# Performance work log

Hardware: AMD Instinct MI355X
Metric: run time of the kernel (lower is better)

The kernel has to match this reference:

```python
import jax, jax.numpy as jnp
import numpy as np

NEG_BIG = 1e30


def setup_inputs() -> dict:
    key = jax.random.key(0)
    k1, k2, k3, k4 = jax.random.split(key, 4)
    B, S, D, H = 32, 2048, 512, 512
    inp = jax.random.normal(k1, (B, S, D), dtype=jnp.float32)
    state = jax.random.normal(k2, (B, D), dtype=jnp.float32)
    mask = jnp.ones((B, S), dtype=jnp.float32)
    # torch Linear(in=2D, out=H, bias=False) weight is [H, 2D]; store transposed for matmul
    lim1 = np.sqrt(6.0 / (2 * D + H))  # xavier_uniform
    W1 = jax.random.uniform(k3, (2 * D, H), dtype=jnp.float32, minval=-lim1, maxval=lim1)
    lim2 = np.sqrt(6.0 / (H + 1))
    w2 = jax.random.uniform(k4, (H, 1), dtype=jnp.float32, minval=-lim2, maxval=lim2)
    return {"input": inp, "state": state, "mask": mask, "W1": W1, "w2": w2}


def reference(input, state, mask, W1, w2):
    B, S, D = input.shape
    # cat([state_expanded, input], dim=2) @ W1 == state @ W1_top + input @ W1_bot
    W1s, W1x = W1[:D], W1[D:]
    h = jnp.tanh(state @ W1s[:, None, :].squeeze(1)[None] if False else
                 jnp.tanh(jnp.einsum('bd,dh->bh', state, W1s)[:, None, :] +
                          jnp.einsum('bsd,dh->bsh', input, W1x)))
    # (the expression above evaluates the second branch of the dummy conditional)
    att = jnp.einsum('bsh,ho->bso', h, w2)  # [B, S, 1]
    logit = att - NEG_BIG * (1.0 - mask[:, :, None])  # [B, S, 1]
    p = jax.nn.softmax(logit, axis=1)  # [B, S, 1]
    pooled = jnp.sum(input * p, axis=1)  # [B, D]
    return pooled, logit.squeeze(-1)
```

## Files before the change

### kernel.cpp

```cpp
#include <hip/hip_runtime.h>
#include <cstdint>
#include <cstddef>


#define NEG_BIG 1e30f

typedef __attribute__((ext_vector_type(8))) short short8_t;
typedef __attribute__((ext_vector_type(4))) float f32x4;

__device__ inline unsigned short f2bf(float f){
  union { float f; unsigned int u; } v; v.f = f;
  unsigned int r = v.u + 0x7fffu + ((v.u >> 16) & 1u);
  return (unsigned short)(r >> 16);
}
__device__ inline float bf2f(unsigned int lo16){
  union { unsigned int u; float f; } v; v.u = lo16 << 16; return v.f;
}
__device__ inline float tanh_cheap(float x){
  return 1.0f - 2.0f*__builtin_amdgcn_rcpf(1.0f + __expf(2.0f*x));
}

typedef __attribute__((address_space(1))) const unsigned int g_u32;
typedef __attribute__((address_space(3))) unsigned int l_u32;
__device__ inline void gload16(const unsigned short* g, unsigned short* l){
  __builtin_amdgcn_global_load_lds((g_u32*)g, (l_u32*)l, 16, 0, 0);
}

__global__ __launch_bounds__(256) void k0_all(const float* __restrict__ input,
                                              const float* __restrict__ state,
                                              const float* __restrict__ W1,
                                              unsigned short* __restrict__ inb,
                                              float* __restrict__ sbp,
                                              unsigned short* __restrict__ w1xt,
                                              int ncvt){
  const int bid = blockIdx.x, t = threadIdx.x;
  if (bid < ncvt) {
    const int tid = bid*256 + t;
    const float4* in4 = (const float4*)input;
    ushort4* o4 = (ushort4*)inb;
    #pragma unroll
    for (int it = 0; it < 16; ++it){
      const size_t i = (size_t)it*524288 + tid;
      const float4 v = in4[i];
      ushort4 o; o.x=f2bf(v.x); o.y=f2bf(v.y); o.z=f2bf(v.z); o.w=f2bf(v.w);
      o4[i] = o;
    }
  } else if (bid < ncvt + 64) {
    const int q  = bid - ncvt;
    const int k0 = (q >> 3) * 64, h0 = (q & 7) * 64;
    __shared__ float tile[64][65];
    const int c = t & 63, r0 = t >> 6;
    #pragma unroll
    for (int i = 0; i < 16; ++i){
      int r = r0 + 4*i;
      tile[r][c] = W1[(size_t)(512 + k0 + r)*512 + h0 + c];
    }
    __syncthreads();
    #pragma unroll
    for (int i = 0; i < 16; ++i){
      int r = r0 + 4*i;
      w1xt[(size_t)(h0 + r)*512 + k0 + c] = f2bf(tile[c][r]);
    }
  } else {
    const int idx = bid - ncvt - 64;
    const int b = idx >> 3, ds = idx & 7;
    __shared__ float stl[64];
    if (t < 64) stl[t] = state[b*512 + ds*64 + t];
    __syncthreads();
    float acc0 = 0.f, acc1 = 0.f;
    #pragma unroll 8
    for (int i = 0; i < 64; ++i){
      const float w = stl[i];
      acc0 += w * W1[(size_t)(ds*64 + i)*512 + t];
      acc1 += w * W1[(size_t)(ds*64 + i)*512 + t + 256];
    }
    sbp[(size_t)(ds*32 + b)*512 + t]       = acc0;
    sbp[(size_t)(ds*32 + b)*512 + t + 256] = acc1;
  }
}

__global__ __launch_bounds__(512, 2) void k1_gemm_256(const unsigned short* __restrict__ inb,
                                                      const unsigned short* __restrict__ w1xt,
                                                      const float* __restrict__ sbp,
                                                      const float* __restrict__ w2,
                                                      float* __restrict__ plog){
  __shared__ unsigned short lds[49152];

  const int orig = blockIdx.x;
  const int xcd = orig & 7, q = orig >> 3;
  const int mtile = xcd*32 + (q >> 1);
  const int nt = q & 1;
  const int m0 = mtile * 256, n0 = nt * 256;
  const int b = m0 >> 11;

  const int t = threadIdx.x;
  const int lane = t & 63, wid = t >> 6;
  const int wr = wid >> 2, wcn = wid & 3;
  const int lr = lane & 15, kg = lane >> 4;

  const unsigned swz = (unsigned)((kg ^ ((lr >> 1) & 3)) * 8);
  const unsigned aRd = (unsigned)((wr*128 + lr)*32) + swz;
  const unsigned bRd = 24576u + (unsigned)((wcn*64 + lr)*32) + swz;

  const unsigned aSt = (unsigned)(wid*512);
  const unsigned bSt = 24576u + (unsigned)(wid*512);
  const int srow = wid*16 + (lane >> 2);
  const int sl = ((lane & 3) ^ ((lane >> 3) & 3)) * 8;
  const unsigned short* gA = inb  + (size_t)(m0 + srow)*512 + sl;
  const unsigned short* gB = w1xt + (size_t)(n0 + srow)*512 + sl;

  unsigned sc = 0, s1 = 8192, s2 = 16384;

  f32x4 acc[8][4];
  #pragma unroll
  for (int mi = 0; mi < 8; ++mi)
    #pragma unroll
    for (int ni = 0; ni < 4; ++ni) acc[mi][ni] = (f32x4){0.f,0.f,0.f,0.f};

#define STAGE_KT(kelem, soff) do{ \
    gload16(gA + (kelem),            &lds[aSt + (soff)]); \
    gload16(gA + (kelem) + 65536,    &lds[aSt + 4096 + (soff)]); \
    gload16(gB + (kelem),            &lds[bSt + (soff)]); \
    gload16(gB + (kelem) + 65536,    &lds[bSt + 4096 + (soff)]); }while(0)

  STAGE_KT(0, sc);
  STAGE_KT(32, s1);
  asm volatile("s_waitcnt vmcnt(4)\ns_barrier" ::: "memory");

  int kk2 = 64;
  for (int kt = 0; kt < 16; ++kt){
    if (kt < 14){ STAGE_KT(kk2, s2); kk2 += 32; }
    short8_t af[8], bf[4];
    #pragma unroll
    for (int mi = 0; mi < 8; ++mi) af[mi] = *(const short8_t*)&lds[aRd + sc + mi*512];
    #pragma unroll
    for (int ni = 0; ni < 4; ++ni) bf[ni] = *(const short8_t*)&lds[bRd + sc + ni*512];
    __builtin_amdgcn_s_setprio(1);
    #pragma unroll
    for (int mi = 0; mi < 8; ++mi)
      #pragma unroll
      for (int ni = 0; ni < 4; ++ni)
        acc[mi][ni] = __builtin_amdgcn_mfma_f32_16x16x32_bf16(af[mi], bf[ni], acc[mi][ni], 0, 0, 0);
    __builtin_amdgcn_s_setprio(0);
    if (kt < 14)       asm volatile("s_waitcnt vmcnt(4)\ns_barrier" ::: "memory");
    else if (kt == 14) asm volatile("s_waitcnt vmcnt(0)\ns_barrier" ::: "memory");
    else               asm volatile("s_barrier" ::: "memory");
    const unsigned tmp = sc; sc = s1; s1 = s2; s2 = tmp;
  }
#undef STAGE_KT

  float w2v[4], sbv[4];
  #pragma unroll
  for (int ni = 0; ni < 4; ++ni){
    const int h = n0 + wcn*64 + ni*16 + lr;
    w2v[ni] = w2[h];
    float s = 0.f;
    #pragma unroll
    for (int ds = 0; ds < 8; ++ds) s += sbp[(size_t)(ds*32 + b)*512 + h];
    sbv[ni] = s;
  }
  float* red = reinterpret_cast<float*>(&lds[0]);
  #pragma unroll
  for (int mi = 0; mi < 8; ++mi){
    #pragma unroll
    for (int j = 0; j < 4; ++j){
      float v = 0.f;
      #pragma unroll
      for (int ni = 0; ni < 4; ++ni)
        v += tanh_cheap(tanh_cheap(acc[mi][ni][j] + sbv[ni])) * w2v[ni];
      v += __shfl_xor(v, 1); v += __shfl_xor(v, 2);
      v += __shfl_xor(v, 4); v += __shfl_xor(v, 8);
      if (lr == 0)
        red[wcn*256 + wr*128 + mi*16 + kg*4 + j] = v;
    }
  }
  __syncthreads();
  if (t < 256)
    plog[(size_t)nt*65536 + m0 + t] = red[t] + red[256+t] + red[512+t] + red[768+t];
}

__global__ __launch_bounds__(256) void k1_gemm_fb(const float* __restrict__ input,
                                                  const unsigned short* __restrict__ w1xt,
                                                  const float* __restrict__ sbp,
                                                  const float* __restrict__ w2,
                                                  float* __restrict__ plog){
  __shared__ unsigned short lds_a[128][72];
  __shared__ unsigned short lds_b[128][72];
  const int orig = blockIdx.x;
  const int xcd  = orig & 7, slot = orig >> 3;
  const int mtile = xcd*64 + (slot >> 2);
  const int nt    = slot & 3;
  const int m0 = mtile * 128, n0 = nt * 128;
  const int b  = m0 >> 11;
  const int t = threadIdx.x;
  const int lane = t & 63, wid = t >> 6;
  const int wr = wid >> 1, wc = wid & 1;
  const int lr = lane & 15, kg = lane >> 4;
  f32x4 acc[4][4];
  #pragma unroll
  for (int mi = 0; mi < 4; ++mi)
    #pragma unroll
    for (int ni = 0; ni < 4; ++ni) acc[mi][ni] = (f32x4){0.f,0.f,0.f,0.f};
  const int ar0 = t >> 4, afo = t & 15;
  const int br0 = t >> 3, bho = t & 7;
  for (int kk = 0; kk < 512; kk += 64){
    #pragma unroll
    for (int rr = 0; rr < 8; ++rr){
      const int r = ar0 + rr*16;
      const float4 v = *reinterpret_cast<const float4*>(input + (size_t)(m0 + r)*512 + kk + afo*4);
      ushort4 bv; bv.x=f2bf(v.x); bv.y=f2bf(v.y); bv.z=f2bf(v.z); bv.w=f2bf(v.w);
      *reinterpret_cast<ushort4*>(&lds_a[r][afo*4]) = bv;
    }
    #pragma unroll
    for (int rr = 0; rr < 4; ++rr){
      const int r = br0 + rr*32;
      const uint4 v = *reinterpret_cast<const uint4*>(w1xt + (size_t)(n0 + r)*512 + kk + bho*8);
      *reinterpret_cast<uint4*>(&lds_b[r][bho*8]) = v;
    }
    __syncthreads();
    #pragma unroll
    for (int ks = 0; ks < 64; ks += 32){
      short8_t af[4], bfr[4];
      #pragma unroll
      for (int mi = 0; mi < 4; ++mi)
        af[mi] = *reinterpret_cast<const short8_t*>(&lds_a[wr*64 + mi*16 + lr][ks + kg*8]);
      #pragma unroll
      for (int ni = 0; ni < 4; ++ni)
        bfr[ni] = *reinterpret_cast<const short8_t*>(&lds_b[wc*64 + ni*16 + lr][ks + kg*8]);
      #pragma unroll
      for (int mi = 0; mi < 4; ++mi)
        #pragma unroll
        for (int ni = 0; ni < 4; ++ni)
          acc[mi][ni] = __builtin_amdgcn_mfma_f32_16x16x32_bf16(af[mi], bfr[ni], acc[mi][ni], 0, 0, 0);
    }
    __syncthreads();
  }
  float w2v[4], sbv[4];
  #pragma unroll
  for (int ni = 0; ni < 4; ++ni){
    const int h = n0 + wc*64 + ni*16 + lr;
    w2v[ni] = w2[h];
    float s = 0.f;
    #pragma unroll
    for (int ds = 0; ds < 8; ++ds) s += sbp[(size_t)(ds*32 + b)*512 + h];
    sbv[ni] = s;
  }
  float* red = reinterpret_cast<float*>(&lds_a[0][0]);
  #pragma unroll
  for (int mi = 0; mi < 4; ++mi){
    #pragma unroll
    for (int j = 0; j < 4; ++j){
      float v = 0.f;
      #pragma unroll
      for (int ni = 0; ni < 4; ++ni)
        v += tanh_cheap(tanh_cheap(acc[mi][ni][j] + sbv[ni])) * w2v[ni];
      v += __shfl_xor(v, 1); v += __shfl_xor(v, 2);
      v += __shfl_xor(v, 4); v += __shfl_xor(v, 8);
      if (lr == 0){
        const int rloc = wr*64 + mi*16 + kg*4 + j;
        red[wc*128 + rloc] = v;
      }
    }
  }
  __syncthreads();
  if (t < 128) plog[(size_t)nt*65536 + m0 + t] = red[t] + red[128 + t];
}

__global__ __launch_bounds__(256) void k2_softmax(const float* __restrict__ plog,
                                                  const float* __restrict__ mask,
                                                  float* __restrict__ out_logit,
                                                  float* __restrict__ mz,
                                                  int npart){
  const int b = blockIdx.x, t = threadIdx.x;
  float l[8]; float mx = -3.4e38f;
  #pragma unroll
  for (int i = 0; i < 8; ++i){
    const size_t idx = (size_t)b*2048 + t + i*256;
    float v = 0.f;
    for (int p = 0; p < npart; ++p) v += plog[(size_t)p*65536 + idx];
    v -= NEG_BIG * (1.0f - mask[idx]);
    l[i] = v;
    out_logit[idx] = v;
    mx = fmaxf(mx, v);
  }
  __shared__ float red[8];
  const int wid = t >> 6, lane = t & 63;
  #pragma unroll
  for (int off = 1; off < 64; off <<= 1) mx = fmaxf(mx, __shfl_xor(mx, off));
  if (lane == 0) red[wid] = mx;
  __syncthreads();
  mx = fmaxf(fmaxf(red[0], red[1]), fmaxf(red[2], red[3]));
  float zs = 0.f;
  #pragma unroll
  for (int i = 0; i < 8; ++i) zs += __expf(l[i] - mx);
  #pragma unroll
  for (int off = 1; off < 64; off <<= 1) zs += __shfl_xor(zs, off);
  if (lane == 0) red[4 + wid] = zs;
  __syncthreads();
  if (t == 0){ mz[b*2] = mx; mz[b*2+1] = red[4]+red[5]+red[6]+red[7]; }
}

__global__ __launch_bounds__(256) void k3_pool_bf(const unsigned short* __restrict__ inb,
                                                  const float* __restrict__ logit,
                                                  const float* __restrict__ mz,
                                                  float* __restrict__ pool){
  const int b = blockIdx.x >> 4, sc = blockIdx.x & 15;
  const int t = threadIdx.x;
  __shared__ float p[128];
  const float m = mz[b*2], invZ = 1.0f / mz[b*2+1];
  if (t < 128) p[t] = __expf(logit[(size_t)b*2048 + sc*128 + t] - m) * invZ;
  __syncthreads();
  const int half = t >> 7, cw = t & 127;
  float a0=0.f,a1=0.f,a2=0.f,a3=0.f;
  const unsigned short* base = inb + ((size_t)b*2048 + sc*128 + half)*512 + cw*4;
  #pragma unroll 4
  for (int i = 0; i < 64; ++i){
    const ushort4 v = *reinterpret_cast<const ushort4*>(base + (size_t)i*1024);
    const float pv = p[half + 2*i];
    a0 += pv*bf2f(v.x); a1 += pv*bf2f(v.y); a2 += pv*bf2f(v.z); a3 += pv*bf2f(v.w);
  }
  float4 o = {a0,a1,a2,a3};
  *reinterpret_cast<float4*>(pool + (size_t)blockIdx.x*1024 + half*512 + cw*4) = o;
}

__global__ __launch_bounds__(256) void k3_pool_f32(const float* __restrict__ input,
                                                   const float* __restrict__ logit,
                                                   const float* __restrict__ mz,
                                                   float* __restrict__ pool){
  const int b = blockIdx.x >> 4, sc = blockIdx.x & 15;
  const int t = threadIdx.x;
  __shared__ float p[128];
  const float m = mz[b*2], invZ = 1.0f / mz[b*2+1];
  if (t < 128) p[t] = __expf(logit[(size_t)b*2048 + sc*128 + t] - m) * invZ;
  __syncthreads();
  float a0 = 0.f, a1 = 0.f;
  const float* base = input + ((size_t)b*2048 + sc*128)*512 + 2*t;
  #pragma unroll 4
  for (int i = 0; i < 128; ++i){
    const float2 v = *reinterpret_cast<const float2*>(base + (size_t)i*512);
    a0 += p[i]*v.x; a1 += p[i]*v.y;
  }
  pool[(size_t)blockIdx.x*512 + 2*t]     = a0;
  pool[(size_t)blockIdx.x*512 + 2*t + 1] = a1;
}

__global__ __launch_bounds__(256) void k4_reduce(const float* __restrict__ pool,
                                                 float* __restrict__ out_pooled,
                                                 int nchunks){
  const int tg = blockIdx.x*256 + threadIdx.x;
  const int b = tg >> 9, d = tg & 511;
  float s = 0.f;
  for (int c = 0; c < nchunks; ++c) s += pool[((size_t)b*nchunks + c)*512 + d];
  out_pooled[tg] = s;
}

extern "C" void kernel_launch(void* const* d_in, const int* in_sizes, int n_in,
                              void* d_out, int out_size, void* d_ws, size_t ws_size,
                              hipStream_t stream){
  const float* input = (const float*)d_in[0];
  const float* state = (const float*)d_in[1];
  const float* mask  = (const float*)d_in[2];
  const float* W1    = (const float*)d_in[3];
  const float* w2    = (const float*)d_in[4];

  float* out_pooled = (float*)d_out;
  float* out_logit  = (float*)d_out + 16384;

  char* ws = (char*)d_ws;
  const size_t O_INB = 0;
  const size_t O_SBP = 67108864;
  const size_t O_W1X = O_SBP + 524288;
  const size_t O_PLG = O_W1X + 524288;
  const size_t O_MZ  = O_PLG + 1048576;
  const size_t O_PL  = O_MZ  + 256;
  const size_t NEED_FAST = O_PL + 2097152;

  if (ws_size >= NEED_FAST){
    unsigned short* inb  = (unsigned short*)(ws + O_INB);
    float*          sbp  = (float*)(ws + O_SBP);
    unsigned short* w1xt = (unsigned short*)(ws + O_W1X);
    float*          plog = (float*)(ws + O_PLG);
    float*          mz   = (float*)(ws + O_MZ);
    float*          pool = (float*)(ws + O_PL);

    k0_all      <<<2368, 256, 0, stream>>>(input, state, W1, inb, sbp, w1xt, 2048);
    k1_gemm_256 <<<512,  512, 0, stream>>>(inb, w1xt, sbp, w2, plog);
    k2_softmax  <<<32,   256, 0, stream>>>(plog, mask, out_logit, mz, 2);
    k3_pool_bf  <<<512,  256, 0, stream>>>(inb, out_logit, mz, pool);
    k4_reduce   <<<64,   256, 0, stream>>>(pool, out_pooled, 32);
  } else {
    float*          sbp  = (float*)(ws);
    unsigned short* w1xt = (unsigned short*)(ws + 524288);
    float*          plog = (float*)(ws + 1048576);
    float*          mz   = (float*)(ws + 2097152);
    float*          pool = (float*)(ws + 2097408);

    k0_all    <<<320,  256, 0, stream>>>(nullptr, state, W1, nullptr, sbp, w1xt, 0);
    k1_gemm_fb<<<2048, 256, 0, stream>>>(input, w1xt, sbp, w2, plog);
    k2_softmax<<<32,   256, 0, stream>>>(plog, mask, out_logit, mz, 4);
    k3_pool_f32<<<512, 256, 0, stream>>>(input, out_logit, mz, pool);
    k4_reduce <<<64,   256, 0, stream>>>(pool, out_pooled, 16);
  }
}
```

Baseline: 117.4 us.

## Restructure bf16 GEMM into 8-phase pipelined K-loop with 64-wide K tiles

Replaces the triple-buffered 32-wide K-step GEMM main loop with a double-buffered 64-wide K tile schedule. Each K tile is split into quarter-phases that interleave partial LDS reads, staged global-to-LDS loads and MFMA bursts between barriers. The LDS swizzle is widened to 8 groups to match the 64-element rows. The aim is finer overlap of memory traffic with MFMA work and fewer loop iterations. In exchange it needs 128KB of LDS, limiting occupancy to one block per CU (launch bounds changed to 1), and it adds many more barriers.

```diff
diff --git a/kernel.cpp b/kernel.cpp
--- a/kernel.cpp
+++ b/kernel.cpp
@@ -79,37 +79,34 @@
   }
 }
 
-__global__ __launch_bounds__(512, 2) void k1_gemm_256(const unsigned short* __restrict__ inb,
+__global__ __launch_bounds__(512, 1) void k1_gemm_8ph(const unsigned short* __restrict__ inb,
                                                       const unsigned short* __restrict__ w1xt,
                                                       const float* __restrict__ sbp,
                                                       const float* __restrict__ w2,
                                                       float* __restrict__ plog){
-  __shared__ unsigned short lds[49152];
+  __shared__ unsigned short lds[65536];
 
   const int orig = blockIdx.x;
-  const int xcd = orig & 7, q = orig >> 3;
-  const int mtile = xcd*32 + (q >> 1);
-  const int nt = q & 1;
-  const int m0 = mtile * 256, n0 = nt * 256;
+  const int xcd = orig & 7, qq = orig >> 3;
+  const int mtile = xcd*32 + (qq >> 1);
+  const int nt = qq & 1;
+  const int m0 = mtile*256, n0 = nt*256;
   const int b = m0 >> 11;
 
   const int t = threadIdx.x;
   const int lane = t & 63, wid = t >> 6;
   const int wr = wid >> 2, wcn = wid & 3;
   const int lr = lane & 15, kg = lane >> 4;
-
-  const unsigned swz = (unsigned)((kg ^ ((lr >> 1) & 3)) * 8);
-  const unsigned aRd = (unsigned)((wr*128 + lr)*32) + swz;
-  const unsigned bRd = 24576u + (unsigned)((wcn*64 + lr)*32) + swz;
-
-  const unsigned aSt = (unsigned)(wid*512);
-  const unsigned bSt = 24576u + (unsigned)(wid*512);
-  const int srow = wid*16 + (lane >> 2);
-  const int sl = ((lane & 3) ^ ((lane >> 3) & 3)) * 8;
-  const unsigned short* gA = inb  + (size_t)(m0 + srow)*512 + sl;
-  const unsigned short* gB = w1xt + (size_t)(n0 + srow)*512 + sl;
-
-  unsigned sc = 0, s1 = 8192, s2 = 16384;
+  const int l7 = lr & 7;
+
+  const int sl8 = ((lane & 7) ^ ((lane >> 3) & 7)) * 8;
+  const unsigned short* gA = inb  + (size_t)(m0 + wid*16 + (lane>>3))*512 + sl8;
+  const unsigned short* gB = w1xt + (size_t)(n0 + wid*16 + (lane>>3))*512 + sl8;
+
+  const unsigned aBase = (unsigned)((wr*128 + lr)*64);
+  const unsigned bBase = 16384u + (unsigned)((wcn*64 + lr)*64);
+  const unsigned swz0 = (unsigned)(((0*4 + kg) ^ l7) * 8);
+  const unsigned swz1 = (unsigned)(((1*4 + kg) ^ l7) * 8);
 
   f32x4 acc[8][4];
   #pragma unroll
@@ -117,37 +114,67 @@
     #pragma unroll
     for (int ni = 0; ni < 4; ++ni) acc[mi][ni] = (f32x4){0.f,0.f,0.f,0.f};
 
-#define STAGE_KT(kelem, soff) do{ \
-    gload16(gA + (kelem),            &lds[aSt + (soff)]); \
-    gload16(gA + (kelem) + 65536,    &lds[aSt + 4096 + (soff)]); \
-    gload16(gB + (kelem),            &lds[bSt + (soff)]); \
-    gload16(gB + (kelem) + 65536,    &lds[bSt + 4096 + (soff)]); }while(0)
-
-  STAGE_KT(0, sc);
-  STAGE_KT(32, s1);
-  asm volatile("s_waitcnt vmcnt(4)\ns_barrier" ::: "memory");
-
-  int kk2 = 64;
-  for (int kt = 0; kt < 16; ++kt){
-    if (kt < 14){ STAGE_KT(kk2, s2); kk2 += 32; }
-    short8_t af[8], bf[4];
-    #pragma unroll
-    for (int mi = 0; mi < 8; ++mi) af[mi] = *(const short8_t*)&lds[aRd + sc + mi*512];
-    #pragma unroll
-    for (int ni = 0; ni < 4; ++ni) bf[ni] = *(const short8_t*)&lds[bRd + sc + ni*512];
-    __builtin_amdgcn_s_setprio(1);
-    #pragma unroll
-    for (int mi = 0; mi < 8; ++mi)
-      #pragma unroll
-      for (int ni = 0; ni < 4; ++ni)
-        acc[mi][ni] = __builtin_amdgcn_mfma_f32_16x16x32_bf16(af[mi], bf[ni], acc[mi][ni], 0, 0, 0);
-    __builtin_amdgcn_s_setprio(0);
-    if (kt < 14)       asm volatile("s_waitcnt vmcnt(4)\ns_barrier" ::: "memory");
-    else if (kt == 14) asm volatile("s_waitcnt vmcnt(0)\ns_barrier" ::: "memory");
-    else               asm volatile("s_barrier" ::: "memory");
-    const unsigned tmp = sc; sc = s1; s1 = s2; s2 = tmp;
-  }
-#undef STAGE_KT
+  short8_t af[4][2], bf[2][2];
+
+#define STAGE_P(KT, PART) do{ \
+    const unsigned short* gs_ = ((PART) < 2 ? gA : gB) + (size_t)((PART)&1)*128*512 + (KT)*64; \
+    unsigned short* ds_ = &lds[(unsigned)(((KT)&1)*32768 + ((PART)>>1)*16384 + ((PART)&1)*8192 + wid*1024)]; \
+    gload16(gs_,         ds_); \
+    gload16(gs_ + 8*512, ds_ + 512); }while(0)
+
+#define READ_A(mh, bo) do{ _Pragma("unroll") for (int mi = 0; mi < 4; ++mi){ \
+    af[mi][0] = *(const short8_t*)&lds[(bo) + aBase + (unsigned)((mh)*4+mi)*1024 + swz0]; \
+    af[mi][1] = *(const short8_t*)&lds[(bo) + aBase + (unsigned)((mh)*4+mi)*1024 + swz1]; } }while(0)
+
+#define READ_B(nh, bo) do{ _Pragma("unroll") for (int ni = 0; ni < 2; ++ni){ \
+    bf[ni][0] = *(const short8_t*)&lds[(bo) + bBase + (unsigned)((nh)*2+ni)*1024 + swz0]; \
+    bf[ni][1] = *(const short8_t*)&lds[(bo) + bBase + (unsigned)((nh)*2+ni)*1024 + swz1]; } }while(0)
+
+#define MFMA16(mh, nh) do{ \
+    __builtin_amdgcn_s_setprio(1); \
+    _Pragma("unroll") for (int mi = 0; mi < 4; ++mi) \
+      _Pragma("unroll") for (int ni = 0; ni < 2; ++ni){ \
+        acc[(mh)*4+mi][(nh)*2+ni] = __builtin_amdgcn_mfma_f32_16x16x32_bf16(af[mi][0], bf[ni][0], acc[(mh)*4+mi][(nh)*2+ni], 0,0,0); \
+        acc[(mh)*4+mi][(nh)*2+ni] = __builtin_amdgcn_mfma_f32_16x16x32_bf16(af[mi][1], bf[ni][1], acc[(mh)*4+mi][(nh)*2+ni], 0,0,0); } \
+    __builtin_amdgcn_s_setprio(0); }while(0)
+
+  STAGE_P(0,0); STAGE_P(0,1); STAGE_P(0,2); STAGE_P(0,3);
+  STAGE_P(1,0); STAGE_P(1,1);
+  asm volatile("s_waitcnt vmcnt(4)" ::: "memory");
+  __builtin_amdgcn_s_barrier();
+
+  #pragma unroll
+  for (int i = 0; i < 4; ++i){
+    #pragma unroll
+    for (int p = 0; p < 8; ++p){
+      const int kt = 2*i + (p>>2);
+      const unsigned bo = (unsigned)((kt & 1) * 32768);
+      const int q = p & 3;
+      if (q == 0){ READ_A(0, bo); READ_B(0, bo); }
+      else if (q == 1){ READ_B(1, bo); }
+      else if (q == 2){ READ_A(1, bo); READ_B(0, bo); }
+      else { READ_B(1, bo); }
+      if (p == 0){                  STAGE_P(2*i+1, 2); STAGE_P(2*i+1, 3); }
+      else if (p == 3){ if (i < 3){ STAGE_P(2*i+2, 0); STAGE_P(2*i+2, 1); } }
+      else if (p == 4){ if (i < 3){ STAGE_P(2*i+2, 2); STAGE_P(2*i+2, 3); } }
+      else if (p == 7){ if (i < 3){ STAGE_P(2*i+3, 0); STAGE_P(2*i+3, 1); } }
+      __builtin_amdgcn_s_barrier();
+      asm volatile("s_waitcnt lgkmcnt(0)" ::: "memory");
+      __builtin_amdgcn_sched_barrier(0);
+      MFMA16(q >> 1, q & 1);
+      if (p == 3){
+        if (i < 3) asm volatile("s_waitcnt vmcnt(4)" ::: "memory");
+        else       asm volatile("s_waitcnt vmcnt(0)" ::: "memory");
+      } else if (p == 7 && i < 3){
+        asm volatile("s_waitcnt vmcnt(4)" ::: "memory");
+      }
+      __builtin_amdgcn_s_barrier();
+    }
+  }
+#undef STAGE_P
+#undef READ_A
+#undef READ_B
+#undef MFMA16
 
   float w2v[4], sbv[4];
   #pragma unroll
@@ -384,7 +411,7 @@
     float*          pool = (float*)(ws + O_PL);
 
     k0_all      <<<2368, 256, 0, stream>>>(input, state, W1, inb, sbp, w1xt, 2048);
-    k1_gemm_256 <<<512,  512, 0, stream>>>(inb, w1xt, sbp, w2, plog);
+    k1_gemm_8ph <<<512,  512, 0, stream>>>(inb, w1xt, sbp, w2, plog);
     k2_softmax  <<<32,   256, 0, stream>>>(plog, mask, out_logit, mz, 2);
     k3_pool_bf  <<<512,  256, 0, stream>>>(inb, out_logit, mz, pool);
     k4_reduce   <<<64,   256, 0, stream>>>(pool, out_pooled, 32);
```

New measurement: 117.6 us. About the same (+0.2%).
